# Kernel optimization log

Hardware: AMD Instinct MI355X
Metric: run time of the kernel (lower is better)

The kernel has to match this reference:

```python
import jax, jax.numpy as jnp
import numpy as np

N_NODES = 100000
N_EDGES = 1600000
IN_F, HID, OUT_F, K = 64, 64, 16, 3


def gcn_conv(x, src, dst, deg_inv_sqrt, W, b):
    """One PyG-style GCNConv with precomputed self-loop-augmented edges & norm.
    x: [N, Fin]; src/dst: [E+N]; W: [Fin, Fout]; b: [Fout]."""
    h = x @ W                                  # [N, Fout]
    norm = deg_inv_sqrt[src] * deg_inv_sqrt[dst]  # [E+N]
    msg = h[src] * norm[:, None]               # gather + scale  [E+N, Fout]
    out = jax.ops.segment_sum(msg, dst, num_segments=x.shape[0])  # scatter-add
    return out + b


def _prep_edges(edge_index, n):
    loop = jnp.arange(n, dtype=edge_index.dtype)
    src = jnp.concatenate([edge_index[0], loop])
    dst = jnp.concatenate([edge_index[1], loop])
    deg = jax.ops.segment_sum(jnp.ones_like(dst, dtype=jnp.float32), dst, num_segments=n)
    deg_inv_sqrt = jnp.where(deg > 0, jax.lax.rsqrt(jnp.maximum(deg, 1.0)), 0.0)
    return src, dst, deg_inv_sqrt


def setup_inputs() -> dict:
    key = jax.random.key(0)
    ks = jax.random.split(key, 10)
    x = jax.random.normal(ks[0], (N_NODES, IN_F), dtype=jnp.float32)
    edge_index = jax.random.randint(ks[1], (2, N_EDGES), 0, N_NODES, dtype=jnp.int32)
    # Glorot-ish init for weights, zeros for biases (PyG default)
    def glorot(k, fin, fout):
        s = float(np.sqrt(6.0 / (fin + fout)))
        return jax.random.uniform(k, (fin, fout), jnp.float32, -s, s)
    W_in = glorot(ks[2], IN_F, HID)
    b_in = jnp.zeros((HID,), jnp.float32)
    W_h = jnp.stack([glorot(ks[3 + i], HID, HID) for i in range(K - 1)])  # [K-1, HID, HID]
    b_h = jnp.zeros((K - 1, HID), jnp.float32)
    W_out = glorot(ks[3 + K], HID, OUT_F)
    b_out = jnp.zeros((OUT_F,), jnp.float32)
    return {"x": x, "edge_index": edge_index, "W_in": W_in, "b_in": b_in,
            "W_h": W_h, "b_h": b_h, "W_out": W_out, "b_out": b_out}


def reference(x, edge_index, W_in, b_in, W_h, b_h, W_out, b_out):
    src, dst, dis = _prep_edges(edge_index, x.shape[0])
    h = jax.nn.relu(gcn_conv(x, src, dst, dis, W_in, b_in))
    for i in range(W_h.shape[0]):
        h = jax.nn.relu(gcn_conv(h, src, dst, dis, W_h[i], b_h[i]))
    return gcn_conv(h, src, dst, dis, W_out, b_out)
```

## Files before the change

kernel.cpp:

```cpp
#include <hip/hip_runtime.h>


#define BKT_SHIFT 7
#define BKT_NODES 128
#define NBMAX 800
#define CAP 4096
#define EPT 16

typedef __attribute__((ext_vector_type(8))) short short8;
typedef __attribute__((ext_vector_type(4))) float f32x4;

union U4S8 { uint4 u; short8 s; };
__device__ __forceinline__ short8 as_s8(uint4 u) { U4S8 c; c.u = u; return c.s; }

__device__ __forceinline__ unsigned bf16rne(float f) {
    unsigned u = __float_as_uint(f);
    return (u + 0x7FFFu + ((u >> 16) & 1u)) >> 16;
}
__device__ __forceinline__ unsigned pack2(float a, float b) {
    return bf16rne(a) | (bf16rne(b) << 16);
}
__device__ __forceinline__ float lo16(unsigned u) { return __uint_as_float(u << 16); }
__device__ __forceinline__ float hi16(unsigned u) { return __uint_as_float(u & 0xFFFF0000u); }

__global__ void k_prep(const float* __restrict__ W_in, const float* __restrict__ W_h,
                       const float* __restrict__ W_out, unsigned short* __restrict__ Wt,
                       int* __restrict__ gcursor, int nb) {
    int i = blockIdx.x * 256 + threadIdx.x;
    if (i < 12288) {
        int w = i >> 12, r = i & 4095;
        int col = r >> 6, k = r & 63;
        const float* Wp = (w == 0) ? W_in : W_h + (size_t)(w - 1) * 4096;
        Wt[i] = (unsigned short)bf16rne(Wp[(size_t)k * 64 + col]);
    } else if (i < 13312) {
        int r = i - 12288;
        int col = r >> 6, k = r & 63;
        Wt[i] = (unsigned short)bf16rne(W_out[(size_t)k * 16 + col]);
    }
    if (i < nb) gcursor[i] = i * CAP;
}

__global__ __launch_bounds__(256) void k_binB(const int* __restrict__ src,
                                              const int* __restrict__ dst, int e, int nb,
                                              int* __restrict__ gcursor,
                                              unsigned* __restrict__ bkt_edges) {
    __shared__ int lcnt[NBMAX];
    __shared__ int lbase[NBMAX];
    int tdx = threadIdx.x;
    for (int i = tdx; i < nb; i += 256) lcnt[i] = 0;
    __syncthreads();
    int base = blockIdx.x * (256 * EPT);
    unsigned val[EPT];
    int bkt[EPT];
#pragma unroll
    for (int k = 0; k < EPT; ++k) {
        int i = base + k * 256 + tdx;
        if (i < e) {
            int s_ = src[i], d_ = dst[i];
            val[k] = ((unsigned)s_ << BKT_SHIFT) | (unsigned)(d_ & (BKT_NODES - 1));
            bkt[k] = d_ >> BKT_SHIFT;
            atomicAdd(&lcnt[bkt[k]], 1);
        } else bkt[k] = -1;
    }
    __syncthreads();
    for (int b = tdx; b < nb; b += 256) {
        int c = lcnt[b];
        lbase[b] = c ? atomicAdd(&gcursor[b], c) : 0;
        lcnt[b] = 0;
    }
    __syncthreads();
#pragma unroll
    for (int k = 0; k < EPT; ++k) {
        if (bkt[k] >= 0) {
            int o = atomicAdd(&lcnt[bkt[k]], 1);
            bkt_edges[lbase[bkt[k]] + o] = val[k];
        }
    }
}

__global__ __launch_bounds__(256) void k_bsort(
    const int* __restrict__ gcursor, const unsigned* __restrict__ bkt_edges,
    int* __restrict__ row_beg, int* __restrict__ row_end, int* __restrict__ csr_src,
    float* __restrict__ dis, int n) {
    __shared__ int hist[BKT_NODES];
    __shared__ int sc[BKT_NODES];
    __shared__ int cur[BKT_NODES];
    int b = blockIdx.x, tdx = threadIdx.x;
    int beg = b * CAP;
    int end = gcursor[b];
    if (tdx < BKT_NODES) hist[tdx] = 0;
    __syncthreads();
    for (int j = beg + tdx; j < end; j += 256)
        atomicAdd(&hist[bkt_edges[j] & (BKT_NODES - 1)], 1);
    __syncthreads();
    if (tdx < BKT_NODES) sc[tdx] = hist[tdx];
    __syncthreads();
    for (int off = 1; off < BKT_NODES; off <<= 1) {
        int v = (tdx < BKT_NODES && tdx >= off) ? sc[tdx - off] : 0;
        __syncthreads();
        if (tdx < BKT_NODES && tdx >= off) sc[tdx] += v;
        __syncthreads();
    }
    if (tdx < BKT_NODES) {
        int node = b * BKT_NODES + tdx;
        if (node < n) {
            int pos = beg + sc[tdx] - hist[tdx];
            row_beg[node] = pos;
            row_end[node] = pos + hist[tdx];
            cur[tdx] = pos;
            dis[node] = rsqrtf((float)(hist[tdx] + 1));
        }
    }
    __syncthreads();
    for (int j = beg + tdx; j < end; j += 256) {
        unsigned ev = bkt_edges[j];
        int p = atomicAdd(&cur[ev & (BKT_NODES - 1)], 1);
        csr_src[p] = (int)(ev >> BKT_SHIFT);
    }
}

__global__ __launch_bounds__(256) void k_mmfma_x(
    const float4* __restrict__ x4,
    const uint4* __restrict__ Wt,
    const float* __restrict__ dis,
    unsigned short* __restrict__ t, int n) {
    int wave = threadIdx.x >> 6, lane = threadIdx.x & 63;
    int base = blockIdx.x * 64 + wave * 16;
    if (base >= n) return;
    int l15 = lane & 15, lq = lane >> 4;

    int arow = base + l15;
    int ac = arow < n ? arow : n - 1;
    const float4* xr = x4 + (size_t)ac * 16;
    float4 f0 = xr[lq * 2], f1 = xr[lq * 2 + 1];
    float4 f2 = xr[8 + lq * 2], f3 = xr[9 + lq * 2];
    uint4 u0, u1;
    u0.x = pack2(f0.x, f0.y); u0.y = pack2(f0.z, f0.w);
    u0.z = pack2(f1.x, f1.y); u0.w = pack2(f1.z, f1.w);
    u1.x = pack2(f2.x, f2.y); u1.y = pack2(f2.z, f2.w);
    u1.z = pack2(f3.x, f3.y); u1.w = pack2(f3.z, f3.w);
    short8 a0 = as_s8(u0), a1 = as_s8(u1);

    int orow0 = base + lq * 4;
    float dn[4];
#pragma unroll
    for (int r = 0; r < 4; ++r) {
        int rr = orow0 + r;
        dn[r] = (rr < n) ? dis[rr] : 0.f;
    }
#pragma unroll
    for (int c = 0; c < 4; ++c) {
        short8 b0 = as_s8(Wt[(size_t)(c * 16 + l15) * 8 + lq]);
        short8 b1 = as_s8(Wt[(size_t)(c * 16 + l15) * 8 + 4 + lq]);
        f32x4 acc = {0.f, 0.f, 0.f, 0.f};
        acc = __builtin_amdgcn_mfma_f32_16x16x32_bf16(a0, b0, acc, 0, 0, 0);
        acc = __builtin_amdgcn_mfma_f32_16x16x32_bf16(a1, b1, acc, 0, 0, 0);
#pragma unroll
        for (int r = 0; r < 4; ++r) {
            int row = orow0 + r;
            if (row < n)
                t[(size_t)row * 64 + c * 16 + l15] = (unsigned short)bf16rne(acc[r] * dn[r]);
        }
    }
}

#define ACC4(v) \
    acc.x += lo16(v.x); acc.y += hi16(v.x); acc.z += lo16(v.y); acc.w += hi16(v.y);

template<int NC>
__global__ __launch_bounds__(256) void k_fused(
    const int* __restrict__ row_beg, const int* __restrict__ row_end,
    const int* __restrict__ csr_src,
    const uint2* __restrict__ t_in,
    const float* __restrict__ dis, const float* __restrict__ bias,
    const uint4* __restrict__ Wt,
    unsigned short* __restrict__ t_out, int n) {
    __shared__ unsigned short htile[64][72];

    int tdx = threadIdx.x;
    int grp = tdx >> 4, l15 = tdx & 15;
    int grpbase = tdx & 48;
    int nblk0 = blockIdx.x * 64;

    const float4 bb = *(const float4*)(bias + l15 * 4);

#pragma unroll
    for (int rnd = 0; rnd < 4; ++rnd) {
        int nl = rnd * 16 + grp;
        int node = nblk0 + nl;
        uint2 hw = make_uint2(0u, 0u);
        if (node < n) {
            int beg = row_beg[node], end = row_end[node];
            uint2 sv0 = t_in[(size_t)node * 16 + l15];
            float4 acc = make_float4(lo16(sv0.x), hi16(sv0.x), lo16(sv0.y), hi16(sv0.y));
            for (int j0 = beg; j0 < end; j0 += 16) {
                int myj = j0 + l15;
                int sv  = (myj < end) ? csr_src[myj] : 0;
                int m   = end - j0; if (m > 16) m = 16;
                int k = 0;
                for (; k + 8 <= m; k += 8) {
                    int s0 = __shfl(sv, grpbase + k);
                    int s1 = __shfl(sv, grpbase + k + 1);
                    int s2 = __shfl(sv, grpbase + k + 2);
                    int s3 = __shfl(sv, grpbase + k + 3);
                    int s4 = __shfl(sv, grpbase + k + 4);
                    int s5 = __shfl(sv, grpbase + k + 5);
                    int s6 = __shfl(sv, grpbase + k + 6);
                    int s7 = __shfl(sv, grpbase + k + 7);
                    uint2 v0 = t_in[(size_t)s0 * 16 + l15];
                    uint2 v1 = t_in[(size_t)s1 * 16 + l15];
                    uint2 v2 = t_in[(size_t)s2 * 16 + l15];
                    uint2 v3 = t_in[(size_t)s3 * 16 + l15];
                    uint2 v4 = t_in[(size_t)s4 * 16 + l15];
                    uint2 v5 = t_in[(size_t)s5 * 16 + l15];
                    uint2 v6 = t_in[(size_t)s6 * 16 + l15];
                    uint2 v7 = t_in[(size_t)s7 * 16 + l15];
                    ACC4(v0) ACC4(v1) ACC4(v2) ACC4(v3)
                    ACC4(v4) ACC4(v5) ACC4(v6) ACC4(v7)
                }
                for (; k < m; ++k) {
                    int s0 = __shfl(sv, grpbase + k);
                    uint2 v0 = t_in[(size_t)s0 * 16 + l15];
                    ACC4(v0)
                }
            }
            float dn = dis[node];
            float ox = fmaxf(fmaf(dn, acc.x, bb.x), 0.f);
            float oy = fmaxf(fmaf(dn, acc.y, bb.y), 0.f);
            float oz = fmaxf(fmaf(dn, acc.z, bb.z), 0.f);
            float ow = fmaxf(fmaf(dn, acc.w, bb.w), 0.f);
            hw = make_uint2(pack2(ox, oy), pack2(oz, ow));
        }
        *(uint2*)&htile[nl][l15 * 4] = hw;
    }
    __syncthreads();

    int wave = tdx >> 6, lane = tdx & 63;
    int lq = lane >> 4;
    int rbase = wave * 16;
    short8 a0 = as_s8(*(const uint4*)&htile[rbase + l15][lq * 8]);
    short8 a1 = as_s8(*(const uint4*)&htile[rbase + l15][32 + lq * 8]);

    int orow0 = nblk0 + rbase + lq * 4;
    float dn[4];
#pragma unroll
    for (int r = 0; r < 4; ++r) {
        int rr = orow0 + r;
        dn[r] = (rr < n) ? dis[rr] : 0.f;
    }
#pragma unroll
    for (int c = 0; c < NC; ++c) {
        short8 b0 = as_s8(Wt[(size_t)(c * 16 + l15) * 8 + lq]);
        short8 b1 = as_s8(Wt[(size_t)(c * 16 + l15) * 8 + 4 + lq]);
        f32x4 acc = {0.f, 0.f, 0.f, 0.f};
        acc = __builtin_amdgcn_mfma_f32_16x16x32_bf16(a0, b0, acc, 0, 0, 0);
        acc = __builtin_amdgcn_mfma_f32_16x16x32_bf16(a1, b1, acc, 0, 0, 0);
#pragma unroll
        for (int r = 0; r < 4; ++r) {
            int row = orow0 + r;
            if (row < n)
                t_out[(size_t)row * (NC * 16) + c * 16 + l15] =
                    (unsigned short)bf16rne(acc[r] * dn[r]);
        }
    }
}

__global__ void k_gather16(const int* __restrict__ row_beg, const int* __restrict__ row_end,
                           const int* __restrict__ csr_src,
                           const uint2* __restrict__ t2, const float* __restrict__ dis,
                           const float* __restrict__ b, float* __restrict__ out, int n) {
    int tid  = blockIdx.x * blockDim.x + threadIdx.x;
    int node = tid >> 2;
    if (node >= n) return;
    int lane3   = threadIdx.x & 3;
    int grpbase = threadIdx.x & 60;
    int beg = row_beg[node], end = row_end[node];

    uint2 sv0 = t2[(size_t)node * 4 + lane3];
    float4 acc = make_float4(lo16(sv0.x), hi16(sv0.x), lo16(sv0.y), hi16(sv0.y));

    for (int j0 = beg; j0 < end; j0 += 4) {
        int myj = j0 + lane3;
        int sv  = (myj < end) ? csr_src[myj] : 0;
        int m   = end - j0; if (m > 4) m = 4;
        int k = 0;
        for (; k + 2 <= m; k += 2) {
            int s0 = __shfl(sv, grpbase + k);
            int s1 = __shfl(sv, grpbase + k + 1);
            uint2 v0 = t2[(size_t)s0 * 4 + lane3];
            uint2 v1 = t2[(size_t)s1 * 4 + lane3];
            ACC4(v0) ACC4(v1)
        }
        for (; k < m; ++k) {
            int s0 = __shfl(sv, grpbase + k);
            uint2 v0 = t2[(size_t)s0 * 4 + lane3];
            ACC4(v0)
        }
    }
    float dn = dis[node];
    const float4 bb = *(const float4*)(b + lane3 * 4);
    float4 o;
    o.x = fmaf(dn, acc.x, bb.x);
    o.y = fmaf(dn, acc.y, bb.y);
    o.z = fmaf(dn, acc.z, bb.z);
    o.w = fmaf(dn, acc.w, bb.w);
    *(float4*)(out + (size_t)node * 16 + lane3 * 4) = o;
}


extern "C" void kernel_launch(void* const* d_in, const int* in_sizes, int n_in,
                              void* d_out, int out_size, void* d_ws, size_t ws_size,
                              hipStream_t stream) {
    const float* x     = (const float*)d_in[0];
    const int*   ei    = (const int*)d_in[1];
    const float* W_in  = (const float*)d_in[2];
    const float* b_in  = (const float*)d_in[3];
    const float* W_h   = (const float*)d_in[4];
    const float* b_h   = (const float*)d_in[5];
    const float* W_out = (const float*)d_in[6];
    const float* b_out = (const float*)d_in[7];

    const int n = in_sizes[0] / 64;
    const int e = in_sizes[1] / 2;
    const int* src = ei;
    const int* dst = ei + e;
    const int nb = (n + BKT_NODES - 1) / BKT_NODES;
    if (nb > NBMAX) return;

    char* ws = (char*)d_ws;
    size_t off = 0;
    auto alloc = [&](size_t bytes) { void* p = ws + off; off += (bytes + 255) & ~(size_t)255; return p; };
    float*          dis       = (float*)alloc((size_t)n * 4);
    unsigned short* t_a       = (unsigned short*)alloc((size_t)n * 64 * 2);
    unsigned short* t_b       = (unsigned short*)alloc((size_t)n * 64 * 2);
    unsigned short* Wt        = (unsigned short*)alloc(13312 * 2);
    int*            gcursor   = (int*)alloc((size_t)nb * 4);
    unsigned*       bkt_edges = (unsigned*)alloc((size_t)nb * CAP * 4);
    int*            row_beg   = (int*)alloc((size_t)n * 4);
    int*            row_end   = (int*)alloc((size_t)n * 4);
    int*            csr_src   = (int*)alloc((size_t)nb * CAP * 4);

    const int nblk_e = (e + 256 * EPT - 1) / (256 * EPT);
    const int nblk_f = (n + 63) / 64;

    k_prep <<<52, 256, 0, stream>>>(W_in, W_h, W_out, Wt, gcursor, nb);
    k_binB <<<nblk_e, 256, 0, stream>>>(src, dst, e, nb, gcursor, bkt_edges);
    k_bsort<<<nb, 256, 0, stream>>>(gcursor, bkt_edges, row_beg, row_end, csr_src, dis, n);

    k_mmfma_x<<<nblk_f, 256, 0, stream>>>((const float4*)x, (const uint4*)Wt, dis, t_a, n);

    k_fused<4><<<nblk_f, 256, 0, stream>>>(row_beg, row_end, csr_src, (const uint2*)t_a,
                                           dis, b_in, (const uint4*)(Wt + 4096), t_b, n);
    k_fused<4><<<nblk_f, 256, 0, stream>>>(row_beg, row_end, csr_src, (const uint2*)t_b,
                                           dis, b_h, (const uint4*)(Wt + 8192), t_a, n);
    k_fused<1><<<nblk_f, 256, 0, stream>>>(row_beg, row_end, csr_src, (const uint2*)t_a,
                                           dis, b_h + 64, (const uint4*)(Wt + 12288), t_b, n);
    k_gather16<<<(n * 4 + 255) / 256, 256, 0, stream>>>(row_beg, row_end, csr_src,
                                                        (const uint2*)t_b, dis, b_out,
                                                        (float*)d_out, n);
}
```

Measured before the change: 201.1 us.

## Gather one node per 8-lane group with 16-byte loads in fused GCN layer

Rewrites the aggregation in the fused gather+matmul kernel. Each 8-lane group now owns one node and each lane loads uint4 (8 bf16 features), instead of 16 lanes looping over four rounds of nodes with uint2 loads. Blocks grow to 512 threads so all 64 nodes of a tile are gathered at once, and the MFMA output columns are split across the two halves of the waves. The intent is wider memory transactions and more independent gathers in flight. The cost is higher per-block register and thread demand, and idle waves in the NC=1 layer.

```diff
diff --git a/kernel.cpp b/kernel.cpp
--- a/kernel.cpp
+++ b/kernel.cpp
@@ -164,80 +164,84 @@
     }
 }
 
-#define ACC4(v) \
-    acc.x += lo16(v.x); acc.y += hi16(v.x); acc.z += lo16(v.y); acc.w += hi16(v.y);
+#define ACC8(v) \
+    acc0.x += lo16(v.x); acc0.y += hi16(v.x); acc0.z += lo16(v.y); acc0.w += hi16(v.y); \
+    acc1.x += lo16(v.z); acc1.y += hi16(v.z); acc1.z += lo16(v.w); acc1.w += hi16(v.w);
 
 template<int NC>
-__global__ __launch_bounds__(256) void k_fused(
+__global__ __launch_bounds__(512) void k_fused(
     const int* __restrict__ row_beg, const int* __restrict__ row_end,
     const int* __restrict__ csr_src,
-    const uint2* __restrict__ t_in,
+    const uint4* __restrict__ t_in4,
     const float* __restrict__ dis, const float* __restrict__ bias,
     const uint4* __restrict__ Wt,
     unsigned short* __restrict__ t_out, int n) {
     __shared__ unsigned short htile[64][72];
 
     int tdx = threadIdx.x;
-    int grp = tdx >> 4, l15 = tdx & 15;
-    int grpbase = tdx & 48;
+    int lane = tdx & 63;
+    int grp = tdx >> 3, l8 = tdx & 7;
+    int grpbase = lane & 56;
     int nblk0 = blockIdx.x * 64;
-
-    const float4 bb = *(const float4*)(bias + l15 * 4);
-
-#pragma unroll
-    for (int rnd = 0; rnd < 4; ++rnd) {
-        int nl = rnd * 16 + grp;
-        int node = nblk0 + nl;
-        uint2 hw = make_uint2(0u, 0u);
-        if (node < n) {
-            int beg = row_beg[node], end = row_end[node];
-            uint2 sv0 = t_in[(size_t)node * 16 + l15];
-            float4 acc = make_float4(lo16(sv0.x), hi16(sv0.x), lo16(sv0.y), hi16(sv0.y));
-            for (int j0 = beg; j0 < end; j0 += 16) {
-                int myj = j0 + l15;
-                int sv  = (myj < end) ? csr_src[myj] : 0;
-                int m   = end - j0; if (m > 16) m = 16;
-                int k = 0;
-                for (; k + 8 <= m; k += 8) {
+    int node = nblk0 + grp;
+
+    uint4 hw = make_uint4(0u, 0u, 0u, 0u);
+    if (node < n) {
+        int beg = row_beg[node], end = row_end[node];
+        uint4 sv0 = t_in4[(size_t)node * 8 + l8];
+        float4 acc0 = make_float4(lo16(sv0.x), hi16(sv0.x), lo16(sv0.y), hi16(sv0.y));
+        float4 acc1 = make_float4(lo16(sv0.z), hi16(sv0.z), lo16(sv0.w), hi16(sv0.w));
+        for (int j0 = beg; j0 < end; j0 += 8) {
+            int myj = j0 + l8;
+            int sv  = (myj < end) ? csr_src[myj] : 0;
+            int m   = end - j0; if (m > 8) m = 8;
+            if (m == 8) {
+                int s0 = __shfl(sv, grpbase + 0);
+                int s1 = __shfl(sv, grpbase + 1);
+                int s2 = __shfl(sv, grpbase + 2);
+                int s3 = __shfl(sv, grpbase + 3);
+                int s4 = __shfl(sv, grpbase + 4);
+                int s5 = __shfl(sv, grpbase + 5);
+                int s6 = __shfl(sv, grpbase + 6);
+                int s7 = __shfl(sv, grpbase + 7);
+                uint4 v0 = t_in4[(size_t)s0 * 8 + l8];
+                uint4 v1 = t_in4[(size_t)s1 * 8 + l8];
+                uint4 v2 = t_in4[(size_t)s2 * 8 + l8];
+                uint4 v3 = t_in4[(size_t)s3 * 8 + l8];
+                uint4 v4 = t_in4[(size_t)s4 * 8 + l8];
+                uint4 v5 = t_in4[(size_t)s5 * 8 + l8];
+                uint4 v6 = t_in4[(size_t)s6 * 8 + l8];
+                uint4 v7 = t_in4[(size_t)s7 * 8 + l8];
+                ACC8(v0) ACC8(v1) ACC8(v2) ACC8(v3)
+                ACC8(v4) ACC8(v5) ACC8(v6) ACC8(v7)
+            } else {
+                for (int k = 0; k < m; ++k) {
                     int s0 = __shfl(sv, grpbase + k);
-                    int s1 = __shfl(sv, grpbase + k + 1);
-                    int s2 = __shfl(sv, grpbase + k + 2);
-                    int s3 = __shfl(sv, grpbase + k + 3);
-                    int s4 = __shfl(sv, grpbase + k + 4);
-                    int s5 = __shfl(sv, grpbase + k + 5);
-                    int s6 = __shfl(sv, grpbase + k + 6);
-                    int s7 = __shfl(sv, grpbase + k + 7);
-                    uint2 v0 = t_in[(size_t)s0 * 16 + l15];
-                    uint2 v1 = t_in[(size_t)s1 * 16 + l15];
-                    uint2 v2 = t_in[(size_t)s2 * 16 + l15];
-                    uint2 v3 = t_in[(size_t)s3 * 16 + l15];
-                    uint2 v4 = t_in[(size_t)s4 * 16 + l15];
-                    uint2 v5 = t_in[(size_t)s5 * 16 + l15];
-                    uint2 v6 = t_in[(size_t)s6 * 16 + l15];
-                    uint2 v7 = t_in[(size_t)s7 * 16 + l15];
-                    ACC4(v0) ACC4(v1) ACC4(v2) ACC4(v3)
-                    ACC4(v4) ACC4(v5) ACC4(v6) ACC4(v7)
-                }
-                for (; k < m; ++k) {
-                    int s0 = __shfl(sv, grpbase + k);
-                    uint2 v0 = t_in[(size_t)s0 * 16 + l15];
-                    ACC4(v0)
+                    uint4 v0 = t_in4[(size_t)s0 * 8 + l8];
+                    ACC8(v0)
                 }
             }
-            float dn = dis[node];
-            float ox = fmaxf(fmaf(dn, acc.x, bb.x), 0.f);
-            float oy = fmaxf(fmaf(dn, acc.y, bb.y), 0.f);
-            float oz = fmaxf(fmaf(dn, acc.z, bb.z), 0.f);
-            float ow = fmaxf(fmaf(dn, acc.w, bb.w), 0.f);
-            hw = make_uint2(pack2(ox, oy), pack2(oz, ow));
-        }
-        *(uint2*)&htile[nl][l15 * 4] = hw;
-    }
-    __syncthreads();
-
-    int wave = tdx >> 6, lane = tdx & 63;
-    int lq = lane >> 4;
-    int rbase = wave * 16;
+        }
+        float dn = dis[node];
+        const float4 bb0 = *(const float4*)(bias + l8 * 8);
+        const float4 bb1 = *(const float4*)(bias + l8 * 8 + 4);
+        float o0 = fmaxf(fmaf(dn, acc0.x, bb0.x), 0.f);
+        float o1 = fmaxf(fmaf(dn, acc0.y, bb0.y), 0.f);
+        float o2 = fmaxf(fmaf(dn, acc0.z, bb0.z), 0.f);
+        float o3 = fmaxf(fmaf(dn, acc0.w, bb0.w), 0.f);
+        float o4 = fmaxf(fmaf(dn, acc1.x, bb1.x), 0.f);
+        float o5 = fmaxf(fmaf(dn, acc1.y, bb1.y), 0.f);
+        float o6 = fmaxf(fmaf(dn, acc1.z, bb1.z), 0.f);
+        float o7 = fmaxf(fmaf(dn, acc1.w, bb1.w), 0.f);
+        hw = make_uint4(pack2(o0, o1), pack2(o2, o3), pack2(o4, o5), pack2(o6, o7));
+    }
+    *(uint4*)&htile[grp][l8 * 8] = hw;
+    __syncthreads();
+
+    int wave = tdx >> 6;
+    int l15 = lane & 15, lq = lane >> 4;
+    int rbase = (wave & 3) * 16;
+    int chalf = wave >> 2;
     short8 a0 = as_s8(*(const uint4*)&htile[rbase + l15][lq * 8]);
     short8 a1 = as_s8(*(const uint4*)&htile[rbase + l15][32 + lq * 8]);
 
@@ -248,22 +252,42 @@
         int rr = orow0 + r;
         dn[r] = (rr < n) ? dis[rr] : 0.f;
     }
-#pragma unroll
-    for (int c = 0; c < NC; ++c) {
-        short8 b0 = as_s8(Wt[(size_t)(c * 16 + l15) * 8 + lq]);
-        short8 b1 = as_s8(Wt[(size_t)(c * 16 + l15) * 8 + 4 + lq]);
-        f32x4 acc = {0.f, 0.f, 0.f, 0.f};
-        acc = __builtin_amdgcn_mfma_f32_16x16x32_bf16(a0, b0, acc, 0, 0, 0);
-        acc = __builtin_amdgcn_mfma_f32_16x16x32_bf16(a1, b1, acc, 0, 0, 0);
-#pragma unroll
-        for (int r = 0; r < 4; ++r) {
-            int row = orow0 + r;
-            if (row < n)
-                t_out[(size_t)row * (NC * 16) + c * 16 + l15] =
-                    (unsigned short)bf16rne(acc[r] * dn[r]);
-        }
-    }
-}
+    if (NC == 4) {
+#pragma unroll
+        for (int ci = 0; ci < 2; ++ci) {
+            int c = chalf * 2 + ci;
+            short8 b0 = as_s8(Wt[(size_t)(c * 16 + l15) * 8 + lq]);
+            short8 b1 = as_s8(Wt[(size_t)(c * 16 + l15) * 8 + 4 + lq]);
+            f32x4 acc = {0.f, 0.f, 0.f, 0.f};
+            acc = __builtin_amdgcn_mfma_f32_16x16x32_bf16(a0, b0, acc, 0, 0, 0);
+            acc = __builtin_amdgcn_mfma_f32_16x16x32_bf16(a1, b1, acc, 0, 0, 0);
+#pragma unroll
+            for (int r = 0; r < 4; ++r) {
+                int row = orow0 + r;
+                if (row < n)
+                    t_out[(size_t)row * 64 + c * 16 + l15] =
+                        (unsigned short)bf16rne(acc[r] * dn[r]);
+            }
+        }
+    } else {
+        if (chalf == 0) {
+            short8 b0 = as_s8(Wt[(size_t)l15 * 8 + lq]);
+            short8 b1 = as_s8(Wt[(size_t)l15 * 8 + 4 + lq]);
+            f32x4 acc = {0.f, 0.f, 0.f, 0.f};
+            acc = __builtin_amdgcn_mfma_f32_16x16x32_bf16(a0, b0, acc, 0, 0, 0);
+            acc = __builtin_amdgcn_mfma_f32_16x16x32_bf16(a1, b1, acc, 0, 0, 0);
+#pragma unroll
+            for (int r = 0; r < 4; ++r) {
+                int row = orow0 + r;
+                if (row < n)
+                    t_out[(size_t)row * 16 + l15] = (unsigned short)bf16rne(acc[r] * dn[r]);
+            }
+        }
+    }
+}
+
+#define ACC4(v) \
+    acc.x += lo16(v.x); acc.y += hi16(v.x); acc.z += lo16(v.y); acc.w += hi16(v.y);
 
 __global__ void k_gather16(const int* __restrict__ row_beg, const int* __restrict__ row_end,
                            const int* __restrict__ csr_src,
@@ -349,11 +373,11 @@
 
     k_mmfma_x<<<nblk_f, 256, 0, stream>>>((const float4*)x, (const uint4*)Wt, dis, t_a, n);
 
-    k_fused<4><<<nblk_f, 256, 0, stream>>>(row_beg, row_end, csr_src, (const uint2*)t_a,
+    k_fused<4><<<nblk_f, 512, 0, stream>>>(row_beg, row_end, csr_src, (const uint4*)t_a,
                                            dis, b_in, (const uint4*)(Wt + 4096), t_b, n);
-    k_fused<4><<<nblk_f, 256, 0, stream>>>(row_beg, row_end, csr_src, (const uint2*)t_b,
+    k_fused<4><<<nblk_f, 512, 0, stream>>>(row_beg, row_end, csr_src, (const uint4*)t_b,
                                            dis, b_h, (const uint4*)(Wt + 8192), t_a, n);
-    k_fused<1><<<nblk_f, 256, 0, stream>>>(row_beg, row_end, csr_src, (const uint2*)t_a,
+    k_fused<1><<<nblk_f, 512, 0, stream>>>(row_beg, row_end, csr_src, (const uint4*)t_a,
                                            dis, b_h + 64, (const uint4*)(Wt + 12288), t_b, n);
     k_gather16<<<(n * 4 + 255) / 256, 256, 0, stream>>>(row_beg, row_end, csr_src,
                                                         (const uint2*)t_b, dis, b_out,
```

New measurement: 220.9 us. +9.9%, slower.
